# Optimization experiments

Hardware: AMD Instinct MI355X
Metric: run time of the kernel (lower is better)

## Reference

```python
import jax, jax.numpy as jnp
import numpy as np

NU, NI, E = 50000, 20000, 400000
IN, HID, OUT = 128, 256, 128
NEG_SLOPE_ATTN = 0.2   # DGL GATConv default
NEG_SLOPE_ACT = 0.01   # F.leaky_relu default
BN_EPS = 1e-5


def setup_inputs() -> dict:
    key = jax.random.key(0)
    ks = jax.random.split(key, 32)
    d = {}
    d["x_user"] = jax.random.normal(ks[0], (NU, IN), jnp.float32)
    d["x_item"] = jax.random.normal(ks[1], (NI, IN), jnp.float32)
    d["eu"] = jax.random.randint(ks[2], (E,), 0, NU, jnp.int32)
    d["ei"] = jax.random.randint(ks[3], (E,), 0, NI, jnp.int32)
    i = 4
    dims = [(IN, 4, 64), (HID, 4, 64), (HID, 4, 64), (HID, 4, 32)]
    for L, (fin, H, dh) in enumerate(dims):
        for rel in ("ui", "iu"):
            d[f"W{L}_{rel}"] = jax.random.normal(ks[i], (fin, H * dh), jnp.float32) * 0.1; i += 1
            d[f"A{L}_{rel}"] = jax.random.normal(ks[i], (2, H, dh), jnp.float32) * 0.1; i += 1
    # BN params: [layer, (gamma,beta), HID]; gamma near 1, beta near 0
    gu = 1.0 + 0.05 * jax.random.normal(ks[i], (3, 1, HID), jnp.float32); i += 1
    bu = 0.05 * jax.random.normal(ks[i], (3, 1, HID), jnp.float32); i += 1
    gi = 1.0 + 0.05 * jax.random.normal(ks[i], (3, 1, HID), jnp.float32); i += 1
    bi = 0.05 * jax.random.normal(ks[i], (3, 1, HID), jnp.float32); i += 1
    d["bn_u"] = jnp.concatenate([gu, bu], axis=1)
    d["bn_i"] = jnp.concatenate([gi, bi], axis=1)
    return d


def _gat(x_src, x_dst, W, A, src, dst, n_dst):
    # Single-relation bipartite GATConv (DGL semantics).
    H, dh = A.shape[1], A.shape[2]
    hs = (x_src @ W).reshape(-1, H, dh)           # [Ns,H,dh]
    hd = (x_dst @ W).reshape(-1, H, dh)           # [Nd,H,dh]
    el = jnp.einsum('nhd,hd->nh', hs, A[0])
    er = jnp.einsum('nhd,hd->nh', hd, A[1])
    e = jax.nn.leaky_relu(el[src] + er[dst], NEG_SLOPE_ATTN)   # [E,H]
    emax = jax.ops.segment_max(e, dst, num_segments=n_dst)
    ee = jnp.exp(e - emax[dst])
    denom = jax.ops.segment_sum(ee, dst, num_segments=n_dst)
    alpha = ee / denom[dst]                       # segment softmax over in-edges
    out = jax.ops.segment_sum(hs[src] * alpha[..., None], dst, num_segments=n_dst)
    return out.reshape(n_dst, H * dh)


def _bn(x, gamma, beta):
    mu = x.mean(axis=0)
    var = x.var(axis=0)   # biased, matches torch BN normalization
    return gamma * (x - mu) * jax.lax.rsqrt(var + BN_EPS) + beta


def reference(x_user, x_item, eu, ei, W0_ui, W0_iu, A0_ui, A0_iu,
              W1_ui, W1_iu, A1_ui, A1_iu, W2_ui, W2_iu, A2_ui, A2_iu,
              W3_ui, W3_iu, A3_ui, A3_iu, bn_u, bn_i):
    Wui = [W0_ui, W1_ui, W2_ui]; Aui = [A0_ui, A1_ui, A2_ui]
    Wiu = [W0_iu, W1_iu, W2_iu]; Aiu = [A0_iu, A1_iu, A2_iu]
    hu, hi = x_user, x_item
    for L in range(3):
        ni = _gat(hu, hi, Wui[L], Aui[L], eu, ei, NI)   # user -> item
        nu = _gat(hi, hu, Wiu[L], Aiu[L], ei, eu, NU)   # item -> user
        nu = _bn(nu, bn_u[L, 0], bn_u[L, 1])
        ni = _bn(ni, bn_i[L, 0], bn_i[L, 1])
        if L == 2:   # last hidden layer uses tanh in non-residual path
            hu, hi = jnp.tanh(nu), jnp.tanh(ni)
        else:
            hu = jax.nn.leaky_relu(nu, NEG_SLOPE_ACT)
            hi = jax.nn.leaky_relu(ni, NEG_SLOPE_ACT)
    out_i = _gat(hu, hi, W3_ui, A3_ui, eu, ei, NI)
    out_u = _gat(hi, hu, W3_iu, A3_iu, ei, eu, NU)
    return jnp.concatenate([out_u, out_i], axis=0)   # [NU+NI, OUT]
```

## Files before the change

kernel.cpp:

```cpp
#include <hip/hip_runtime.h>

#define NUSERS 50000
#define NITEMS 20000
#define NEDGES 400000

typedef _Float16 f16;
typedef __attribute__((ext_vector_type(8))) _Float16 f16x8;
typedef __attribute__((ext_vector_type(4))) _Float16 f16x4;
typedef __attribute__((ext_vector_type(2))) _Float16 f16x2;
typedef __attribute__((ext_vector_type(4))) float f32x4;
typedef __attribute__((ext_vector_type(2))) float f32x2;

__global__ __launch_bounds__(256) void prep2_k(
    const float* __restrict__ Wa, const float* __restrict__ Aa,
    f16* __restrict__ Bta, float* __restrict__ efa,
    const float* __restrict__ Wb, const float* __restrict__ Ab,
    f16* __restrict__ Btb, float* __restrict__ efb,
    int K, int Nw, int dh) {
  __shared__ float lds[32][33];
  int ntile = (K >> 5) * (Nw >> 5);
  int b = blockIdx.x, t = threadIdx.x;
  if (b < 2 * ntile) {
    const float* W = (b < ntile) ? Wa : Wb;
    f16* Bt = (b < ntile) ? Bta : Btb;
    int tt = (b < ntile) ? b : b - ntile;
    int ntc = Nw >> 5;
    int tr = tt / ntc, tc = tt - tr * ntc;
    int tx = t & 31, ty = t >> 5;
#pragma unroll
    for (int p = 0; p < 4; ++p) {
      int k = tr * 32 + ty + p * 8;
      int n = tc * 32 + tx;
      lds[ty + p * 8][tx] = W[(long)k * Nw + n];
    }
    __syncthreads();
#pragma unroll
    for (int p = 0; p < 4; ++p) {
      int n = tc * 32 + ty + p * 8;
      int k = tr * 32 + tx;
      Bt[(long)n * K + k] = (f16)lds[tx][ty + p * 8];
    }
  } else {
    int idx = (b - 2 * ntile) * 256 + t;
    if (idx >= 2 * K * 8) return;
    const float* W = (idx < K * 8) ? Wa : Wb;
    const float* A = (idx < K * 8) ? Aa : Ab;
    float* ef = (idx < K * 8) ? efa : efb;
    int t2 = (idx < K * 8) ? idx : idx - K * 8;
    int j = t2 / (K * 4);
    int r = t2 - j * K * 4;
    int h = r / K, f = r - h * K;
    const float* Aj = A + j * Nw;
    float s = 0.f;
    for (int d = 0; d < dh; ++d) s += W[f * Nw + h * dh + d] * Aj[h * dh + d];
    ef[j * 4 * K + h * K + f] = s;
  }
}

__global__ __launch_bounds__(256) void hgemm2_k(const f16* __restrict__ Aa, const f16* __restrict__ Bta,
                                                f16* __restrict__ Ca, int Ma, int gya,
                                                const f16* __restrict__ Ab, const f16* __restrict__ Btb,
                                                f16* __restrict__ Cb, int Mb,
                                                int N, int K) {
  __shared__ f16 As[128 * 32];
  __shared__ f16 Bs[128 * 32];
  int by = blockIdx.y;
  const f16* A; const f16* Bt; f16* C; int M; int row0;
  if (by < gya) { A = Aa; Bt = Bta; C = Ca; M = Ma; row0 = by * 128; }
  else          { A = Ab; Bt = Btb; C = Cb; M = Mb; row0 = (by - gya) * 128; }
  int tid = threadIdx.x;
  int col0 = blockIdx.x * 128;
  int lane = tid & 63, wv = tid >> 6;
  int wr = (wv & 1) * 64, wc = (wv >> 1) * 64;
  int l16 = lane & 15, q = lane >> 4;
  f32x4 acc[4][4] = {};
  int r = tid >> 2, c8 = (tid & 3) * 8;
  for (int k0 = 0; k0 < K; k0 += 32) {
    int ra = min(row0 + r, M - 1);
    uint4 va = *(const uint4*)&A[(long)ra * K + k0 + c8];
    int ra2 = min(row0 + r + 64, M - 1);
    uint4 va2 = *(const uint4*)&A[(long)ra2 * K + k0 + c8];
    uint4 vb = *(const uint4*)&Bt[(long)(col0 + r) * K + k0 + c8];
    uint4 vb2 = *(const uint4*)&Bt[(long)(col0 + r + 64) * K + k0 + c8];
    *(uint4*)&As[r * 32 + c8] = va;
    *(uint4*)&As[(r + 64) * 32 + c8] = va2;
    *(uint4*)&Bs[r * 32 + c8] = vb;
    *(uint4*)&Bs[(r + 64) * 32 + c8] = vb2;
    __syncthreads();
    f16x8 af[4], bfr[4];
#pragma unroll
    for (int i = 0; i < 4; ++i) {
      af[i] = *(const f16x8*)&As[(wr + i * 16 + l16) * 32 + q * 8];
      bfr[i] = *(const f16x8*)&Bs[(wc + i * 16 + l16) * 32 + q * 8];
    }
#pragma unroll
    for (int i = 0; i < 4; ++i)
#pragma unroll
      for (int j = 0; j < 4; ++j)
        acc[i][j] = __builtin_amdgcn_mfma_f32_16x16x32_f16(af[i], bfr[j], acc[i][j], 0, 0, 0);
    __syncthreads();
  }
#pragma unroll
  for (int i = 0; i < 4; ++i) {
#pragma unroll
    for (int reg = 0; reg < 4; ++reg) {
      int rr = row0 + wr + i * 16 + q * 4 + reg;
      if (rr < M) {
#pragma unroll
        for (int j = 0; j < 4; ++j)
          C[(long)rr * N + col0 + wc + j * 16 + l16] = (f16)acc[i][j][reg];
      }
    }
  }
}

__global__ __launch_bounds__(256) void eler2_k(
    const float* __restrict__ xu, f16* __restrict__ hbu,
    const float* __restrict__ ef_ui, const float* __restrict__ ef_iu,
    float* __restrict__ el_u, float* __restrict__ er_u,
    const float* __restrict__ xi, f16* __restrict__ hbi,
    float* __restrict__ el_i, float* __restrict__ er_i) {
  const int K = 128;
  int wv = threadIdx.x >> 6, lane = threadIdx.x & 63;
  int g = blockIdx.x * 4 + wv;
  const float* x; f16* hb; const float* elf; const float* erf; float* el; float* er; int n;
  if (g < NUSERS)                { x = xu; hb = hbu; elf = ef_ui; erf = ef_iu + 4 * K; el = el_u; er = er_u; n = g; }
  else if (g < NUSERS + NITEMS)  { x = xi; hb = hbi; elf = ef_iu; erf = ef_ui + 4 * K; el = el_i; er = er_i; n = g - NUSERS; }
  else return;
  long base = (long)n * K;
  int c0 = lane * 2;
  f32x2 xv = *(const f32x2*)&x[base + c0];
  f16x2 hv = { (f16)xv[0], (f16)xv[1] };
  *(f16x2*)&hb[base + c0] = hv;
  float p[8];
#pragma unroll
  for (int jj = 0; jj < 8; ++jj) {
    const float* fr = (jj < 4) ? (elf + jj * K) : (erf + (jj - 4) * K);
    f32x2 f2 = *(const f32x2*)&fr[c0];
    p[jj] = xv[0] * f2[0] + xv[1] * f2[1];
  }
#pragma unroll
  for (int off = 32; off; off >>= 1)
#pragma unroll
    for (int jj = 0; jj < 8; ++jj) p[jj] += __shfl_xor(p[jj], off, 64);
  if (lane == 0) {
    *(float4*)&el[n * 4] = make_float4(p[0], p[1], p[2], p[3]);
    *(float4*)&er[n * 4] = make_float4(p[4], p[5], p[6], p[7]);
  }
}

__global__ void hist_k(const int* __restrict__ ei, int* __restrict__ degi,
                       const int* __restrict__ eu, int* __restrict__ degu) {
  int e = blockIdx.x * blockDim.x + threadIdx.x;
  if (e < NEDGES) atomicAdd(&degi[ei[e]], 1);
  else if (e < 2 * NEDGES) atomicAdd(&degu[eu[e - NEDGES]], 1);
}

__global__ __launch_bounds__(256) void scan1_k(const int* __restrict__ deg,
                                               int* __restrict__ bsum, int N) {
  __shared__ int red[256];
  int base = blockIdx.x * 1024, t = threadIdx.x;
  int s = 0;
#pragma unroll
  for (int j = 0; j < 4; ++j) { int i = base + t * 4 + j; s += (i < N) ? deg[i] : 0; }
  red[t] = s; __syncthreads();
  for (int off = 128; off; off >>= 1) { if (t < off) red[t] += red[t + off]; __syncthreads(); }
  if (t == 0) bsum[blockIdx.x] = red[0];
}

__global__ void scan2_k(int* __restrict__ bsum, int nb, int* __restrict__ endp, int endv) {
  if (threadIdx.x == 0) {
    int run = 0;
    for (int i = 0; i < nb; ++i) { int v = bsum[i]; bsum[i] = run; run += v; }
    *endp = endv;
  }
}

__global__ __launch_bounds__(256) void scan3_k(const int* __restrict__ deg,
                                               const int* __restrict__ bsum,
                                               int* __restrict__ rowptr,
                                               int* __restrict__ cur, int N) {
  __shared__ int tsum[256];
  int base = blockIdx.x * 1024, t = threadIdx.x;
  int v[4]; int s = 0;
#pragma unroll
  for (int j = 0; j < 4; ++j) { int i = base + t * 4 + j; v[j] = (i < N) ? deg[i] : 0; s += v[j]; }
  tsum[t] = s; __syncthreads();
  for (int off = 1; off < 256; off <<= 1) {
    int x = (t >= off) ? tsum[t - off] : 0;
    __syncthreads();
    tsum[t] += x;
    __syncthreads();
  }
  int run = bsum[blockIdx.x] + ((t > 0) ? tsum[t - 1] : 0);
#pragma unroll
  for (int j = 0; j < 4; ++j) {
    int i = base + t * 4 + j;
    if (i < N) { rowptr[i] = run; cur[i] = run; }
    run += v[j];
  }
}

__global__ void scat_k(const int* __restrict__ ei, const int* __restrict__ eu,
                       int* __restrict__ cur, int* __restrict__ csrsrc) {
  int e = blockIdx.x * blockDim.x + threadIdx.x;
  if (e < NEDGES) {
    int p = atomicAdd(&cur[ei[e]], 1);
    __builtin_nontemporal_store(eu[e], &csrsrc[p]);
  } else if (e < 2 * NEDGES) {
    int e2 = e - NEDGES;
    int p = atomicAdd(&cur[NITEMS + eu[e2]], 1);
    __builtin_nontemporal_store(ei[e2], &csrsrc[p]);
  }
}

template <int W, int DH, typename OUT>
__global__ __launch_bounds__(256) void agg_k(
    const float* __restrict__ elA, const float* __restrict__ erA,
    const int* __restrict__ rpA, const int* __restrict__ srcA,
    const f16* __restrict__ hsA, OUT* __restrict__ outA, int nA,
    const float* __restrict__ elB, const float* __restrict__ erB,
    const int* __restrict__ rpB, const int* __restrict__ srcB,
    const f16* __restrict__ hsB, OUT* __restrict__ outB, int nB) {
  constexpr int CPL = W >> 6;
  constexpr int SHIFT = (W == 256) ? 9 : 8;
  constexpr bool OF16 = (sizeof(OUT) == 2);
  __shared__ float alds[4][256];
  __shared__ int soff[4][64];
  int wv = threadIdx.x >> 6;
  int g = blockIdx.x * 4 + wv;
  int lane = threadIdx.x & 63;
  const float* el; const float* er; const int* rp; const int* srcv;
  const f16* hs; OUT* outp; int d;
  if (g < nA)           { el = elA; er = erA; rp = rpA; srcv = srcA; hs = hsA; outp = outA; d = g; }
  else if (g < nA + nB) { el = elB; er = erB; rp = rpB; srcv = srcB; hs = hsB; outp = outB; d = g - nA; }
  else return;
  int s0 = rp[d], s1 = rp[d + 1];
  int deg = s1 - s0;
  int c0 = lane * CPL;
  int h = c0 / DH;
  long obase = (long)d * W + c0;
  if (deg == 0) {
#pragma unroll
    for (int q = 0; q < CPL; ++q) outp[obase + q] = (OUT)0.f;
    return;
  }
  const float NEG = -3.0e38f;
  float acc[CPL];
#pragma unroll
  for (int q = 0; q < CPL; ++q) acc[q] = 0.f;
  float inv;

  if (deg <= 64) {
    int hh = lane & 3, p = lane >> 2;
    float er_h = er[d * 4 + hh];
    float vv[4];
    float vmax = NEG;
#pragma unroll
    for (int j = 0; j < 4; ++j) {
      int slot = j * 16 + p;
      vv[j] = NEG;
      if (slot < deg) {
        int sj = srcv[s0 + slot];
        if (hh == 0) soff[wv][slot] = sj << SHIFT;
        float v = el[sj * 4 + hh] + er_h;
        v = v > 0.f ? v : 0.2f * v;
        vv[j] = v;
        vmax = fmaxf(vmax, v);
      }
    }
#pragma unroll
    for (int off = 4; off < 64; off <<= 1) vmax = fmaxf(vmax, __shfl_xor(vmax, off, 64));
    float ssum = 0.f;
#pragma unroll
    for (int j = 0; j < 4; ++j) {
      int slot = j * 16 + p;
      if (slot < deg) {
        float e = expf(vv[j] - vmax);
        alds[wv][slot * 4 + hh] = e;
        ssum += e;
      } else {
        alds[wv][slot * 4 + hh] = 0.f;
        if (hh == 0) soff[wv][slot] = 0;
      }
    }
#pragma unroll
    for (int off = 4; off < 64; off <<= 1) ssum += __shfl_xor(ssum, off, 64);
    float Sh = __shfl(ssum, (lane & ~3) | h, 64);
    inv = 1.0f / Sh;
    const char* hbase = (const char*)hs + (size_t)c0 * sizeof(f16);
    int degp = (deg + 3) & ~3;
    for (int j = 0; j < degp; j += 4) {
      float aj[4]; int oj[4];
#pragma unroll
      for (int u = 0; u < 4; ++u) {
        aj[u] = alds[wv][(j + u) * 4 + h];
        oj[u] = soff[wv][j + u];
      }
      if constexpr (CPL == 4) {
        f16x4 vj[4];
#pragma unroll
        for (int u = 0; u < 4; ++u)
          vj[u] = *(const f16x4*)(hbase + (size_t)(unsigned)oj[u]);
#pragma unroll
        for (int u = 0; u < 4; ++u) {
          acc[0] += aj[u] * (float)vj[u][0];
          acc[1] += aj[u] * (float)vj[u][1];
          acc[2] += aj[u] * (float)vj[u][2];
          acc[3] += aj[u] * (float)vj[u][3];
        }
      } else {
        f16x2 vj[4];
#pragma unroll
        for (int u = 0; u < 4; ++u)
          vj[u] = *(const f16x2*)(hbase + (size_t)(unsigned)oj[u]);
#pragma unroll
        for (int u = 0; u < 4; ++u) {
          acc[0] += aj[u] * (float)vj[u][0];
          acc[1] += aj[u] * (float)vj[u][1];
        }
      }
    }
  } else {
    float4 er4 = *(const float4*)&er[d * 4];
    float m0 = NEG, m1 = NEG, m2 = NEG, m3 = NEG;
    for (int k = s0 + lane; k < s1; k += 64) {
      int s = srcv[k];
      float4 e4 = *(const float4*)&el[s * 4];
      float v;
      v = e4.x + er4.x; v = v > 0.f ? v : 0.2f * v; m0 = fmaxf(m0, v);
      v = e4.y + er4.y; v = v > 0.f ? v : 0.2f * v; m1 = fmaxf(m1, v);
      v = e4.z + er4.z; v = v > 0.f ? v : 0.2f * v; m2 = fmaxf(m2, v);
      v = e4.w + er4.w; v = v > 0.f ? v : 0.2f * v; m3 = fmaxf(m3, v);
    }
#pragma unroll
    for (int off = 32; off; off >>= 1) {
      m0 = fmaxf(m0, __shfl_xor(m0, off, 64));
      m1 = fmaxf(m1, __shfl_xor(m1, off, 64));
      m2 = fmaxf(m2, __shfl_xor(m2, off, 64));
      m3 = fmaxf(m3, __shfl_xor(m3, off, 64));
    }
    float S0 = 0.f, S1 = 0.f, S2 = 0.f, S3 = 0.f;
    for (int k = s0 + lane; k < s1; k += 64) {
      int s = srcv[k];
      float4 e4 = *(const float4*)&el[s * 4];
      float v;
      v = e4.x + er4.x; v = v > 0.f ? v : 0.2f * v; S0 += expf(v - m0);
      v = e4.y + er4.y; v = v > 0.f ? v : 0.2f * v; S1 += expf(v - m1);
      v = e4.z + er4.z; v = v > 0.f ? v : 0.2f * v; S2 += expf(v - m2);
      v = e4.w + er4.w; v = v > 0.f ? v : 0.2f * v; S3 += expf(v - m3);
    }
#pragma unroll
    for (int off = 32; off; off >>= 1) {
      S0 += __shfl_xor(S0, off, 64);
      S1 += __shfl_xor(S1, off, 64);
      S2 += __shfl_xor(S2, off, 64);
      S3 += __shfl_xor(S3, off, 64);
    }
    float mh = h == 0 ? m0 : h == 1 ? m1 : h == 2 ? m2 : m3;
    float Sh = h == 0 ? S0 : h == 1 ? S1 : h == 2 ? S2 : S3;
    float erh = h == 0 ? er4.x : h == 1 ? er4.y : h == 2 ? er4.z : er4.w;
    inv = 1.0f / Sh;
    for (int k = s0; k < s1; ++k) {
      int s = srcv[k];
      float v = el[s * 4 + h] + erh; v = v > 0.f ? v : 0.2f * v;
      float a = expf(v - mh);
      const f16* row = &hs[(long)s * W + c0];
      if constexpr (CPL == 4) {
        f16x4 hv = *(const f16x4*)row;
        acc[0] += a * (float)hv[0]; acc[1] += a * (float)hv[1];
        acc[2] += a * (float)hv[2]; acc[3] += a * (float)hv[3];
      } else {
        f16x2 hv = *(const f16x2*)row;
        acc[0] += a * (float)hv[0]; acc[1] += a * (float)hv[1];
      }
    }
  }
  if constexpr (OF16) {
    if constexpr (CPL == 4) {
      f16x4 o = { (f16)(acc[0] * inv), (f16)(acc[1] * inv), (f16)(acc[2] * inv), (f16)(acc[3] * inv) };
      __builtin_nontemporal_store(o, (f16x4*)&outp[obase]);
    } else {
      f16x2 o = { (f16)(acc[0] * inv), (f16)(acc[1] * inv) };
      __builtin_nontemporal_store(o, (f16x2*)&outp[obase]);
    }
  } else {
    if constexpr (CPL == 4) {
      f32x4 o = { acc[0] * inv, acc[1] * inv, acc[2] * inv, acc[3] * inv };
      __builtin_nontemporal_store(o, (f32x4*)&outp[obase]);
    } else {
      f32x2 o = { acc[0] * inv, acc[1] * inv };
      __builtin_nontemporal_store(o, (f32x2*)&outp[obase]);
    }
  }
}

__global__ __launch_bounds__(256) void bn_stats2_k(const f16* __restrict__ xu, float* __restrict__ su, int Nu, int gU,
                                                   const f16* __restrict__ xi, float* __restrict__ si, int Ni) {
  const int C = 256;
  int b = blockIdx.x;
  const f16* x; float* sums; int N; int r0;
  if (b < gU) { x = xu; sums = su; N = Nu; r0 = b * 64; }
  else        { x = xi; sums = si; N = Ni; r0 = (b - gU) * 64; }
  int c = threadIdx.x;
  int r1 = min(r0 + 64, N);
  float s = 0.f, s2 = 0.f;
  for (int r = r0; r < r1; ++r) {
    float v = (float)x[(long)r * C + c];
    s += v; s2 += v * v;
  }
  atomicAdd(&sums[c], s);
  atomicAdd(&sums[C + c], s2);
}

__global__ __launch_bounds__(256) void bn_fused_k(
    const f16* __restrict__ xu, const float* __restrict__ su, const float* __restrict__ gbu,
    f16* __restrict__ yu, int Nu,
    const f16* __restrict__ xi, const float* __restrict__ si, const float* __restrict__ gbi,
    f16* __restrict__ yi, int Ni,
    const float* __restrict__ efu, const float* __restrict__ efiu,
    float* __restrict__ el_u, float* __restrict__ er_u,
    float* __restrict__ el_i, float* __restrict__ er_i, int act) {
  const int Kn = 256;
  int wv = threadIdx.x >> 6, lane = threadIdx.x & 63;
  int g = blockIdx.x * 4 + wv;
  const f16* x; const float* sums; const float* gb; f16* y; int n; int N;
  const float* elf; const float* erf; float* el; float* er;
  if (g < Nu)           { x = xu; sums = su; gb = gbu; y = yu; n = g; N = Nu; elf = efu;  erf = efiu + 4 * Kn; el = el_u; er = er_u; }
  else if (g < Nu + Ni) { x = xi; sums = si; gb = gbi; y = yi; n = g - Nu; N = Ni; elf = efiu; erf = efu + 4 * Kn;  el = el_i; er = er_i; }
  else return;
  long base = (long)n * 256;
  int c0 = lane * 4;
  f16x4 xv = *(const f16x4*)&x[base + c0];
  float4 sm = *(const float4*)&sums[c0];
  float4 q2 = *(const float4*)&sums[256 + c0];
  float4 gg = *(const float4*)&gb[c0];
  float4 bb = *(const float4*)&gb[256 + c0];
  float ms[4] = { sm.x, sm.y, sm.z, sm.w };
  float qs[4] = { q2.x, q2.y, q2.z, q2.w };
  float gs[4] = { gg.x, gg.y, gg.z, gg.w };
  float bs[4] = { bb.x, bb.y, bb.z, bb.w };
  float inv_n = 1.0f / (float)N;
  float v[4];
  f16x4 ov;
#pragma unroll
  for (int q = 0; q < 4; ++q) {
    float mean = ms[q] * inv_n;
    float var = qs[q] * inv_n - mean * mean;
    float t = gs[q] * ((float)xv[q] - mean) * rsqrtf(var + 1e-5f) + bs[q];
    t = act ? tanhf(t) : (t > 0.f ? t : 0.01f * t);
    v[q] = t;
    ov[q] = (f16)t;
  }
  *(f16x4*)&y[base + c0] = ov;
  float p[8];
#pragma unroll
  for (int jj = 0; jj < 8; ++jj) {
    const float* fr = (jj < 4) ? (elf + jj * Kn) : (erf + (jj - 4) * Kn);
    float4 f4 = *(const float4*)&fr[c0];
    p[jj] = v[0] * f4.x + v[1] * f4.y + v[2] * f4.z + v[3] * f4.w;
  }
#pragma unroll
  for (int off = 32; off; off >>= 1)
#pragma unroll
    for (int jj = 0; jj < 8; ++jj) p[jj] += __shfl_xor(p[jj], off, 64);
  if (lane == 0) {
    *(float4*)&el[n * 4] = make_float4(p[0], p[1], p[2], p[3]);
    *(float4*)&er[n * 4] = make_float4(p[4], p[5], p[6], p[7]);
  }
}

extern "C" void kernel_launch(void* const* d_in, const int* in_sizes, int n_in,
                              void* d_out, int out_size, void* d_ws, size_t ws_size,
                              hipStream_t stream) {
  const float* x_user = (const float*)d_in[0];
  const float* x_item = (const float*)d_in[1];
  const int* eu = (const int*)d_in[2];
  const int* ei = (const int*)d_in[3];
  const float *Wm[4][2], *Am[4][2];
  for (int L = 0; L < 4; ++L) {
    Wm[L][0] = (const float*)d_in[4 + L * 4 + 0];
    Am[L][0] = (const float*)d_in[4 + L * 4 + 1];
    Wm[L][1] = (const float*)d_in[4 + L * 4 + 2];
    Am[L][1] = (const float*)d_in[4 + L * 4 + 3];
  }
  const float* bnu = (const float*)d_in[20];
  const float* bni = (const float*)d_in[21];
  float* out = (float*)d_out;

  const int NALL = NITEMS + NUSERS;

  float* ws = (float*)d_ws;
  size_t o = 0;
  float* el_u = ws + o; o += (size_t)NUSERS * 4;
  float* er_u = ws + o; o += (size_t)NUSERS * 4;
  float* el_i = ws + o; o += (size_t)NITEMS * 4;
  float* er_i = ws + o; o += (size_t)NITEMS * 4;
  float* ef_all[4][2];
  for (int L = 0; L < 4; ++L)
    for (int rl = 0; rl < 2; ++rl) { ef_all[L][rl] = ws + o; o += 2048; }
  f16* hb_u   = (f16*)(ws + o); o += (size_t)NUSERS * 128;
  f16* hb_i   = (f16*)(ws + o); o += (size_t)NITEMS * 128;
  f16* hsb_u  = (f16*)(ws + o); o += (size_t)NUSERS * 128;
  f16* hsb_i  = (f16*)(ws + o); o += (size_t)NITEMS * 128;
  f16* aggh_u = (f16*)(ws + o); o += (size_t)NUSERS * 128;
  f16* aggh_i = (f16*)(ws + o); o += (size_t)NITEMS * 128;
  f16* Bt_all[4][2];
  for (int L = 0; L < 4; ++L) {
    int K = (L == 0) ? 128 : 256;
    int W = (L == 3) ? 128 : 256;
    for (int rl = 0; rl < 2; ++rl) { Bt_all[L][rl] = (f16*)(ws + o); o += (size_t)K * W / 2; }
  }
  float* bns_all = ws + o; o += 3 * 1024;
  int* deg_all    = (int*)(ws + o); o += NALL;
  int* rowptr_all = (int*)(ws + o); o += NALL + 4;
  int* cur_all    = (int*)(ws + o); o += NALL;
  int* bsum       = (int*)(ws + o); o += 256;
  int* csrsrc_all = (int*)(ws + o); o += 2 * NEDGES + 4;

  const int gE2 = (2 * NEDGES + 255) / 256;
  const int nb = (NALL + 1023) / 1024;
  const int gU = (NUSERS + 63) / 64;
  const int gI = (NITEMS + 63) / 64;
  const int gNode = (NALL + 3) / 4;

  hipMemsetAsync(bns_all, 0, (3 * 1024 + NALL) * sizeof(float), stream);
  hist_k<<<dim3(gE2), dim3(256), 0, stream>>>(ei, deg_all, eu, deg_all + NITEMS);
  scan1_k<<<dim3(nb), dim3(256), 0, stream>>>(deg_all, bsum, NALL);
  scan2_k<<<dim3(1), dim3(64), 0, stream>>>(bsum, nb, rowptr_all + NALL, 2 * NEDGES);
  scan3_k<<<dim3(nb), dim3(256), 0, stream>>>(deg_all, bsum, rowptr_all, cur_all, NALL);
  scat_k<<<dim3(gE2), dim3(256), 0, stream>>>(ei, eu, cur_all, csrsrc_all);

  const int* rowptr_i = rowptr_all;
  const int* rowptr_u = rowptr_all + NITEMS;

  for (int L = 0; L < 4; ++L) {
    int K = (L == 0) ? 128 : 256;
    int dh = (L == 3) ? 32 : 64;
    int W = 4 * dh;
    int ntile2 = 2 * (K / 32) * (W / 32);
    int gef = (2 * K * 8 + 255) / 256;
    prep2_k<<<dim3(ntile2 + gef), dim3(256), 0, stream>>>(
        Wm[L][0], Am[L][0], Bt_all[L][0], ef_all[L][0],
        Wm[L][1], Am[L][1], Bt_all[L][1], ef_all[L][1], K, W, dh);
  }

  eler2_k<<<dim3(gNode), dim3(256), 0, stream>>>(
      x_user, hb_u, ef_all[0][0], ef_all[0][1], el_u, er_u,
      x_item, hb_i, el_i, er_i);

  int K = 128;
  const int gAgg = gNode;
  const int gya = (NUSERS + 127) / 128, gyb = (NITEMS + 127) / 128;
  for (int L = 0; L < 4; ++L) {
    const int dh = (L == 3) ? 32 : 64;
    const int W = 4 * dh;

    hgemm2_k<<<dim3(W / 128, gya + gyb), dim3(256), 0, stream>>>(
        hb_u, Bt_all[L][0], hsb_u, NUSERS, gya, hb_i, Bt_all[L][1], hsb_i, NITEMS, W, K);

    if (L < 3) {
      float* su = bns_all + (size_t)L * 1024;
      float* si = su + 512;
      agg_k<256, 64, f16><<<dim3(gAgg), dim3(256), 0, stream>>>(
          el_u, er_i, rowptr_i, csrsrc_all, hsb_u, aggh_i, NITEMS,
          el_i, er_u, rowptr_u, csrsrc_all, hsb_i, aggh_u, NUSERS);
      bn_stats2_k<<<dim3(gU + gI), dim3(256), 0, stream>>>(aggh_u, su, NUSERS, gU, aggh_i, si, NITEMS);
      bn_fused_k<<<dim3(gNode), dim3(256), 0, stream>>>(
          aggh_u, su, bnu + L * 512, hb_u, NUSERS,
          aggh_i, si, bni + L * 512, hb_i, NITEMS,
          ef_all[L + 1][0], ef_all[L + 1][1],
          el_u, er_u, el_i, er_i, L == 2);
      K = 256;
    } else {
      agg_k<128, 32, float><<<dim3(gAgg), dim3(256), 0, stream>>>(
          el_u, er_i, rowptr_i, csrsrc_all, hsb_u, out + (size_t)NUSERS * 128, NITEMS,
          el_i, er_u, rowptr_u, csrsrc_all, hsb_i, out, NUSERS);
    }
  }
}
```

Baseline: 853.6 us.

## Fuse BatchNorm statistics into the aggregation kernel via LDS partial sums

```diff
diff --git a/kernel.cpp b/kernel.cpp
--- a/kernel.cpp
+++ b/kernel.cpp
@@ -206,211 +206,226 @@
   int e = blockIdx.x * blockDim.x + threadIdx.x;
   if (e < NEDGES) {
     int p = atomicAdd(&cur[ei[e]], 1);
-    __builtin_nontemporal_store(eu[e], &csrsrc[p]);
+    csrsrc[p] = eu[e];
   } else if (e < 2 * NEDGES) {
     int e2 = e - NEDGES;
     int p = atomicAdd(&cur[NITEMS + eu[e2]], 1);
-    __builtin_nontemporal_store(ei[e2], &csrsrc[p]);
-  }
-}
-
-template <int W, int DH, typename OUT>
+    csrsrc[p] = ei[e2];
+  }
+}
+
+template <int W, int DH, typename OUT, bool STATS>
 __global__ __launch_bounds__(256) void agg_k(
     const float* __restrict__ elA, const float* __restrict__ erA,
     const int* __restrict__ rpA, const int* __restrict__ srcA,
-    const f16* __restrict__ hsA, OUT* __restrict__ outA, int nA,
+    const f16* __restrict__ hsA, OUT* __restrict__ outA, int nA, float* __restrict__ SA,
     const float* __restrict__ elB, const float* __restrict__ erB,
     const int* __restrict__ rpB, const int* __restrict__ srcB,
-    const f16* __restrict__ hsB, OUT* __restrict__ outB, int nB) {
+    const f16* __restrict__ hsB, OUT* __restrict__ outB, int nB, float* __restrict__ SB) {
   constexpr int CPL = W >> 6;
   constexpr int SHIFT = (W == 256) ? 9 : 8;
   constexpr bool OF16 = (sizeof(OUT) == 2);
   __shared__ float alds[4][256];
   __shared__ int soff[4][64];
+  __shared__ float st[STATS ? 2 : 1][STATS ? 512 : 1];
   int wv = threadIdx.x >> 6;
   int g = blockIdx.x * 4 + wv;
   int lane = threadIdx.x & 63;
+  if constexpr (STATS) {
+    int t = threadIdx.x;
+    st[0][t] = 0.f; st[0][t + 256] = 0.f;
+    st[1][t] = 0.f; st[1][t + 256] = 0.f;
+    __syncthreads();
+  }
   const float* el; const float* er; const int* rp; const int* srcv;
-  const f16* hs; OUT* outp; int d;
-  if (g < nA)           { el = elA; er = erA; rp = rpA; srcv = srcA; hs = hsA; outp = outA; d = g; }
-  else if (g < nA + nB) { el = elB; er = erB; rp = rpB; srcv = srcB; hs = hsB; outp = outB; d = g - nA; }
-  else return;
-  int s0 = rp[d], s1 = rp[d + 1];
-  int deg = s1 - s0;
+  const f16* hs; OUT* outp; int d; int side = 0; bool live = true;
+  if (g < nA)           { el = elA; er = erA; rp = rpA; srcv = srcA; hs = hsA; outp = outA; d = g; side = 0; }
+  else if (g < nA + nB) { el = elB; er = erB; rp = rpB; srcv = srcB; hs = hsB; outp = outB; d = g - nA; side = 1; }
+  else {
+    if constexpr (!STATS) return;
+    live = false; d = 0;
+  }
+  const float NEG = -3.0e38f;
+  float vals[CPL];
+#pragma unroll
+  for (int q = 0; q < CPL; ++q) vals[q] = 0.f;
   int c0 = lane * CPL;
   int h = c0 / DH;
-  long obase = (long)d * W + c0;
-  if (deg == 0) {
-#pragma unroll
-    for (int q = 0; q < CPL; ++q) outp[obase + q] = (OUT)0.f;
-    return;
-  }
-  const float NEG = -3.0e38f;
-  float acc[CPL];
-#pragma unroll
-  for (int q = 0; q < CPL; ++q) acc[q] = 0.f;
-  float inv;
-
-  if (deg <= 64) {
-    int hh = lane & 3, p = lane >> 2;
-    float er_h = er[d * 4 + hh];
-    float vv[4];
-    float vmax = NEG;
-#pragma unroll
-    for (int j = 0; j < 4; ++j) {
-      int slot = j * 16 + p;
-      vv[j] = NEG;
-      if (slot < deg) {
-        int sj = srcv[s0 + slot];
-        if (hh == 0) soff[wv][slot] = sj << SHIFT;
-        float v = el[sj * 4 + hh] + er_h;
-        v = v > 0.f ? v : 0.2f * v;
-        vv[j] = v;
-        vmax = fmaxf(vmax, v);
+  int deg = 0;
+  long obase = 0;
+  if (live) {
+    int s0 = rp[d], s1 = rp[d + 1];
+    deg = s1 - s0;
+    obase = (long)d * W + c0;
+    if (deg == 0) {
+#pragma unroll
+      for (int q = 0; q < CPL; ++q) outp[obase + q] = (OUT)0.f;
+    } else {
+      float acc[CPL];
+#pragma unroll
+      for (int q = 0; q < CPL; ++q) acc[q] = 0.f;
+      float inv;
+      if (deg <= 64) {
+        int hh = lane & 3, p = lane >> 2;
+        float er_h = er[d * 4 + hh];
+        float vv[4];
+        float vmax = NEG;
+#pragma unroll
+        for (int j = 0; j < 4; ++j) {
+          int slot = j * 16 + p;
+          vv[j] = NEG;
+          if (slot < deg) {
+            int sj = srcv[s0 + slot];
+            if (hh == 0) soff[wv][slot] = sj << SHIFT;
+            float v = el[sj * 4 + hh] + er_h;
+            v = v > 0.f ? v : 0.2f * v;
+            vv[j] = v;
+            vmax = fmaxf(vmax, v);
+          }
+        }
+#pragma unroll
+        for (int off = 4; off < 64; off <<= 1) vmax = fmaxf(vmax, __shfl_xor(vmax, off, 64));
+        float ssum = 0.f;
+#pragma unroll
+        for (int j = 0; j < 4; ++j) {
+          int slot = j * 16 + p;
+          if (slot < deg) {
+            float e = expf(vv[j] - vmax);
+            alds[wv][slot * 4 + hh] = e;
+            ssum += e;
+          } else {
+            alds[wv][slot * 4 + hh] = 0.f;
+            if (hh == 0) soff[wv][slot] = 0;
+          }
+        }
+#pragma unroll
+        for (int off = 4; off < 64; off <<= 1) ssum += __shfl_xor(ssum, off, 64);
+        float Sh = __shfl(ssum, (lane & ~3) | h, 64);
+        inv = 1.0f / Sh;
+        const char* hbase = (const char*)hs + (size_t)c0 * sizeof(f16);
+        int degp = (deg + 3) & ~3;
+        for (int j = 0; j < degp; j += 4) {
+          float aj[4]; int oj[4];
+#pragma unroll
+          for (int u = 0; u < 4; ++u) {
+            aj[u] = alds[wv][(j + u) * 4 + h];
+            oj[u] = soff[wv][j + u];
+          }
+          if constexpr (CPL == 4) {
+            f16x4 vj[4];
+#pragma unroll
+            for (int u = 0; u < 4; ++u)
+              vj[u] = *(const f16x4*)(hbase + (size_t)(unsigned)oj[u]);
+#pragma unroll
+            for (int u = 0; u < 4; ++u) {
+              acc[0] += aj[u] * (float)vj[u][0];
+              acc[1] += aj[u] * (float)vj[u][1];
+              acc[2] += aj[u] * (float)vj[u][2];
+              acc[3] += aj[u] * (float)vj[u][3];
+            }
+          } else {
+            f16x2 vj[4];
+#pragma unroll
+            for (int u = 0; u < 4; ++u)
+              vj[u] = *(const f16x2*)(hbase + (size_t)(unsigned)oj[u]);
+#pragma unroll
+            for (int u = 0; u < 4; ++u) {
+              acc[0] += aj[u] * (float)vj[u][0];
+              acc[1] += aj[u] * (float)vj[u][1];
+            }
+          }
+        }
+      } else {
+        float4 er4 = *(const float4*)&er[d * 4];
+        float m0 = NEG, m1 = NEG, m2 = NEG, m3 = NEG;
+        for (int k = s0 + lane; k < s1; k += 64) {
+          int s = srcv[k];
+          float4 e4 = *(const float4*)&el[s * 4];
+          float v;
+          v = e4.x + er4.x; v = v > 0.f ? v : 0.2f * v; m0 = fmaxf(m0, v);
+          v = e4.y + er4.y; v = v > 0.f ? v : 0.2f * v; m1 = fmaxf(m1, v);
+          v = e4.z + er4.z; v = v > 0.f ? v : 0.2f * v; m2 = fmaxf(m2, v);
+          v = e4.w + er4.w; v = v > 0.f ? v : 0.2f * v; m3 = fmaxf(m3, v);
+        }
+#pragma unroll
+        for (int off = 32; off; off >>= 1) {
+          m0 = fmaxf(m0, __shfl_xor(m0, off, 64));
+          m1 = fmaxf(m1, __shfl_xor(m1, off, 64));
+          m2 = fmaxf(m2, __shfl_xor(m2, off, 64));
+          m3 = fmaxf(m3, __shfl_xor(m3, off, 64));
+        }
+        float S0 = 0.f, S1 = 0.f, S2 = 0.f, S3 = 0.f;
+        for (int k = s0 + lane; k < s1; k += 64) {
+          int s = srcv[k];
+          float4 e4 = *(const float4*)&el[s * 4];
+          float v;
+          v = e4.x + er4.x; v = v > 0.f ? v : 0.2f * v; S0 += expf(v - m0);
+          v = e4.y + er4.y; v = v > 0.f ? v : 0.2f * v; S1 += expf(v - m1);
+          v = e4.z + er4.z; v = v > 0.f ? v : 0.2f * v; S2 += expf(v - m2);
+          v = e4.w + er4.w; v = v > 0.f ? v : 0.2f * v; S3 += expf(v - m3);
+        }
+#pragma unroll
+        for (int off = 32; off; off >>= 1) {
+          S0 += __shfl_xor(S0, off, 64);
+          S1 += __shfl_xor(S1, off, 64);
+          S2 += __shfl_xor(S2, off, 64);
+          S3 += __shfl_xor(S3, off, 64);
+        }
+        float mh = h == 0 ? m0 : h == 1 ? m1 : h == 2 ? m2 : m3;
+        float Sh = h == 0 ? S0 : h == 1 ? S1 : h == 2 ? S2 : S3;
+        float erh = h == 0 ? er4.x : h == 1 ? er4.y : h == 2 ? er4.z : er4.w;
+        inv = 1.0f / Sh;
+        for (int k = s0; k < s1; ++k) {
+          int s = srcv[k];
+          float v = el[s * 4 + h] + erh; v = v > 0.f ? v : 0.2f * v;
+          float a = expf(v - mh);
+          const f16* row = &hs[(long)s * W + c0];
+          if constexpr (CPL == 4) {
+            f16x4 hv = *(const f16x4*)row;
+            acc[0] += a * (float)hv[0]; acc[1] += a * (float)hv[1];
+            acc[2] += a * (float)hv[2]; acc[3] += a * (float)hv[3];
+          } else {
+            f16x2 hv = *(const f16x2*)row;
+            acc[0] += a * (float)hv[0]; acc[1] += a * (float)hv[1];
+          }
+        }
       }
-    }
-#pragma unroll
-    for (int off = 4; off < 64; off <<= 1) vmax = fmaxf(vmax, __shfl_xor(vmax, off, 64));
-    float ssum = 0.f;
-#pragma unroll
-    for (int j = 0; j < 4; ++j) {
-      int slot = j * 16 + p;
-      if (slot < deg) {
-        float e = expf(vv[j] - vmax);
-        alds[wv][slot * 4 + hh] = e;
-        ssum += e;
+#pragma unroll
+      for (int q = 0; q < CPL; ++q) vals[q] = acc[q] * inv;
+      if constexpr (OF16) {
+        if constexpr (CPL == 4) {
+          f16x4 o = { (f16)vals[0], (f16)vals[1], (f16)vals[2], (f16)vals[3] };
+          __builtin_nontemporal_store(o, (f16x4*)&outp[obase]);
+        } else {
+          f16x2 o = { (f16)vals[0], (f16)vals[1] };
+          __builtin_nontemporal_store(o, (f16x2*)&outp[obase]);
+        }
       } else {
-        alds[wv][slot * 4 + hh] = 0.f;
-        if (hh == 0) soff[wv][slot] = 0;
+        if constexpr (CPL == 4) {
+          f32x4 o = { vals[0], vals[1], vals[2], vals[3] };
+          __builtin_nontemporal_store(o, (f32x4*)&outp[obase]);
+        } else {
+          f32x2 o = { vals[0], vals[1] };
+          __builtin_nontemporal_store(o, (f32x2*)&outp[obase]);
+        }
       }
     }
-#pragma unroll
-    for (int off = 4; off < 64; off <<= 1) ssum += __shfl_xor(ssum, off, 64);
-    float Sh = __shfl(ssum, (lane & ~3) | h, 64);
-    inv = 1.0f / Sh;
-    const char* hbase = (const char*)hs + (size_t)c0 * sizeof(f16);
-    int degp = (deg + 3) & ~3;
-    for (int j = 0; j < degp; j += 4) {
-      float aj[4]; int oj[4];
-#pragma unroll
-      for (int u = 0; u < 4; ++u) {
-        aj[u] = alds[wv][(j + u) * 4 + h];
-        oj[u] = soff[wv][j + u];
+  }
+  if constexpr (STATS) {
+    if (live) {
+#pragma unroll
+      for (int q = 0; q < CPL; ++q) {
+        atomicAdd(&st[side][c0 + q], vals[q]);
+        atomicAdd(&st[side][256 + c0 + q], vals[q] * vals[q]);
       }
-      if constexpr (CPL == 4) {
-        f16x4 vj[4];
-#pragma unroll
-        for (int u = 0; u < 4; ++u)
-          vj[u] = *(const f16x4*)(hbase + (size_t)(unsigned)oj[u]);
-#pragma unroll
-        for (int u = 0; u < 4; ++u) {
-          acc[0] += aj[u] * (float)vj[u][0];
-          acc[1] += aj[u] * (float)vj[u][1];
-          acc[2] += aj[u] * (float)vj[u][2];
-          acc[3] += aj[u] * (float)vj[u][3];
-        }
-      } else {
-        f16x2 vj[4];
-#pragma unroll
-        for (int u = 0; u < 4; ++u)
-          vj[u] = *(const f16x2*)(hbase + (size_t)(unsigned)oj[u]);
-#pragma unroll
-        for (int u = 0; u < 4; ++u) {
-          acc[0] += aj[u] * (float)vj[u][0];
-          acc[1] += aj[u] * (float)vj[u][1];
-        }
-      }
-    }
-  } else {
-    float4 er4 = *(const float4*)&er[d * 4];
-    float m0 = NEG, m1 = NEG, m2 = NEG, m3 = NEG;
-    for (int k = s0 + lane; k < s1; k += 64) {
-      int s = srcv[k];
-      float4 e4 = *(const float4*)&el[s * 4];
-      float v;
-      v = e4.x + er4.x; v = v > 0.f ? v : 0.2f * v; m0 = fmaxf(m0, v);
-      v = e4.y + er4.y; v = v > 0.f ? v : 0.2f * v; m1 = fmaxf(m1, v);
-      v = e4.z + er4.z; v = v > 0.f ? v : 0.2f * v; m2 = fmaxf(m2, v);
-      v = e4.w + er4.w; v = v > 0.f ? v : 0.2f * v; m3 = fmaxf(m3, v);
-    }
-#pragma unroll
-    for (int off = 32; off; off >>= 1) {
-      m0 = fmaxf(m0, __shfl_xor(m0, off, 64));
-      m1 = fmaxf(m1, __shfl_xor(m1, off, 64));
-      m2 = fmaxf(m2, __shfl_xor(m2, off, 64));
-      m3 = fmaxf(m3, __shfl_xor(m3, off, 64));
-    }
-    float S0 = 0.f, S1 = 0.f, S2 = 0.f, S3 = 0.f;
-    for (int k = s0 + lane; k < s1; k += 64) {
-      int s = srcv[k];
-      float4 e4 = *(const float4*)&el[s * 4];
-      float v;
-      v = e4.x + er4.x; v = v > 0.f ? v : 0.2f * v; S0 += expf(v - m0);
-      v = e4.y + er4.y; v = v > 0.f ? v : 0.2f * v; S1 += expf(v - m1);
-      v = e4.z + er4.z; v = v > 0.f ? v : 0.2f * v; S2 += expf(v - m2);
-      v = e4.w + er4.w; v = v > 0.f ? v : 0.2f * v; S3 += expf(v - m3);
-    }
-#pragma unroll
-    for (int off = 32; off; off >>= 1) {
-      S0 += __shfl_xor(S0, off, 64);
-      S1 += __shfl_xor(S1, off, 64);
-      S2 += __shfl_xor(S2, off, 64);
-      S3 += __shfl_xor(S3, off, 64);
-    }
-    float mh = h == 0 ? m0 : h == 1 ? m1 : h == 2 ? m2 : m3;
-    float Sh = h == 0 ? S0 : h == 1 ? S1 : h == 2 ? S2 : S3;
-    float erh = h == 0 ? er4.x : h == 1 ? er4.y : h == 2 ? er4.z : er4.w;
-    inv = 1.0f / Sh;
-    for (int k = s0; k < s1; ++k) {
-      int s = srcv[k];
-      float v = el[s * 4 + h] + erh; v = v > 0.f ? v : 0.2f * v;
-      float a = expf(v - mh);
-      const f16* row = &hs[(long)s * W + c0];
-      if constexpr (CPL == 4) {
-        f16x4 hv = *(const f16x4*)row;
-        acc[0] += a * (float)hv[0]; acc[1] += a * (float)hv[1];
-        acc[2] += a * (float)hv[2]; acc[3] += a * (float)hv[3];
-      } else {
-        f16x2 hv = *(const f16x2*)row;
-        acc[0] += a * (float)hv[0]; acc[1] += a * (float)hv[1];
-      }
-    }
-  }
-  if constexpr (OF16) {
-    if constexpr (CPL == 4) {
-      f16x4 o = { (f16)(acc[0] * inv), (f16)(acc[1] * inv), (f16)(acc[2] * inv), (f16)(acc[3] * inv) };
-      __builtin_nontemporal_store(o, (f16x4*)&outp[obase]);
-    } else {
-      f16x2 o = { (f16)(acc[0] * inv), (f16)(acc[1] * inv) };
-      __builtin_nontemporal_store(o, (f16x2*)&outp[obase]);
-    }
-  } else {
-    if constexpr (CPL == 4) {
-      f32x4 o = { acc[0] * inv, acc[1] * inv, acc[2] * inv, acc[3] * inv };
-      __builtin_nontemporal_store(o, (f32x4*)&outp[obase]);
-    } else {
-      f32x2 o = { acc[0] * inv, acc[1] * inv };
-      __builtin_nontemporal_store(o, (f32x2*)&outp[obase]);
-    }
-  }
-}
-
-__global__ __launch_bounds__(256) void bn_stats2_k(const f16* __restrict__ xu, float* __restrict__ su, int Nu, int gU,
-                                                   const f16* __restrict__ xi, float* __restrict__ si, int Ni) {
-  const int C = 256;
-  int b = blockIdx.x;
-  const f16* x; float* sums; int N; int r0;
-  if (b < gU) { x = xu; sums = su; N = Nu; r0 = b * 64; }
-  else        { x = xi; sums = si; N = Ni; r0 = (b - gU) * 64; }
-  int c = threadIdx.x;
-  int r1 = min(r0 + 64, N);
-  float s = 0.f, s2 = 0.f;
-  for (int r = r0; r < r1; ++r) {
-    float v = (float)x[(long)r * C + c];
-    s += v; s2 += v * v;
-  }
-  atomicAdd(&sums[c], s);
-  atomicAdd(&sums[C + c], s2);
+    }
+    __syncthreads();
+    int t = threadIdx.x;
+    float a0 = st[0][t], a0q = st[0][256 + t];
+    float a1 = st[1][t], a1q = st[1][256 + t];
+    if (a0 != 0.f || a0q != 0.f) { atomicAdd(&SA[t], a0); atomicAdd(&SA[256 + t], a0q); }
+    if (a1 != 0.f || a1q != 0.f) { atomicAdd(&SB[t], a1); atomicAdd(&SB[256 + t], a1q); }
+  }
 }
 
 __global__ __launch_bounds__(256) void bn_fused_k(
@@ -520,8 +535,6 @@
 
   const int gE2 = (2 * NEDGES + 255) / 256;
   const int nb = (NALL + 1023) / 1024;
-  const int gU = (NUSERS + 63) / 64;
-  const int gI = (NITEMS + 63) / 64;
   const int gNode = (NALL + 3) / 4;
 
   hipMemsetAsync(bns_all, 0, (3 * 1024 + NALL) * sizeof(float), stream);
@@ -562,10 +575,9 @@
     if (L < 3) {
       float* su = bns_all + (size_t)L * 1024;
       float* si = su + 512;
-      agg_k<256, 64, f16><<<dim3(gAgg), dim3(256), 0, stream>>>(
-          el_u, er_i, rowptr_i, csrsrc_all, hsb_u, aggh_i, NITEMS,
-          el_i, er_u, rowptr_u, csrsrc_all, hsb_i, aggh_u, NUSERS);
-      bn_stats2_k<<<dim3(gU + gI), dim3(256), 0, stream>>>(aggh_u, su, NUSERS, gU, aggh_i, si, NITEMS);
+      agg_k<256, 64, f16, true><<<dim3(gAgg), dim3(256), 0, stream>>>(
+          el_u, er_i, rowptr_i, csrsrc_all, hsb_u, aggh_i, NITEMS, si,
+          el_i, er_u, rowptr_u, csrsrc_all, hsb_i, aggh_u, NUSERS, su);
       bn_fused_k<<<dim3(gNode), dim3(256), 0, stream>>>(
           aggh_u, su, bnu + L * 512, hb_u, NUSERS,
           aggh_i, si, bni + L * 512, hb_i, NITEMS,
@@ -573,9 +585,9 @@
           el_u, er_u, el_i, er_i, L == 2);
       K = 256;
     } else {
-      agg_k<128, 32, float><<<dim3(gAgg), dim3(256), 0, stream>>>(
-          el_u, er_i, rowptr_i, csrsrc_all, hsb_u, out + (size_t)NUSERS * 128, NITEMS,
-          el_i, er_u, rowptr_u, csrsrc_all, hsb_i, out, NUSERS);
-    }
-  }
-}
+      agg_k<128, 32, float, false><<<dim3(gAgg), dim3(256), 0, stream>>>(
+          el_u, er_i, rowptr_i, csrsrc_all, hsb_u, out + (size_t)NUSERS * 128, NITEMS, nullptr,
+          el_i, er_u, rowptr_u, csrsrc_all, hsb_i, out, NUSERS, nullptr);
+    }
+  }
+}
```

Measured after the change: 1.786 ms. 2.09x slower.
